# Performance work log

Hardware: AMD Instinct MI355X
Metric: run time of the kernel (lower is better)

## Reference

```python
import jax, jax.numpy as jnp
import numpy as np

N_TOKENS, D_MODEL, D_FF, N_EXPERTS, TOP_K = 4096, 2048, 1408, 8, 2


def setup_inputs() -> dict:
    key = jax.random.key(0)
    ks = jax.random.split(key, 6)
    s = 0.02
    return {
        "x": jax.random.normal(ks[0], (N_TOKENS, D_MODEL), jnp.float32),
        "topK_indices": jax.random.randint(ks[1], (N_TOKENS, TOP_K), 0, N_EXPERTS, jnp.int32),
        "topK_scores": jax.random.uniform(ks[2], (N_TOKENS, TOP_K), jnp.float32),
        "W_gate": jax.random.normal(ks[3], (N_EXPERTS, D_MODEL, D_FF), jnp.float32) * s,
        "W_up": jax.random.normal(ks[4], (N_EXPERTS, D_MODEL, D_FF), jnp.float32) * s,
        "W_down": jax.random.normal(ks[5], (N_EXPERTS, D_FF, D_MODEL), jnp.float32) * s,
    }


def reference(x, topK_indices, topK_scores, W_gate, W_up, W_down):
    # Combine weights: combine[n, e] = sum over k of score[n, k] where idx[n, k] == e.
    # Mathematically identical to the torch sort/split/index_add dispatch-combine
    # (with multiply_gate_scores=True), expressed densely for a clean jax baseline.
    n = x.shape[0]
    rows = jnp.arange(n)[:, None]  # [N, 1]
    combine = jnp.zeros((n, W_gate.shape[0]), x.dtype).at[rows, topK_indices].add(topK_scores)
    # Per-expert SwiGLU MLP (llama-moe LinearGLUExperts, bias-free).
    h = jax.nn.silu(jnp.einsum("nd,edh->enh", x, W_gate)) * jnp.einsum("nd,edh->enh", x, W_up)
    expert_out = jnp.einsum("enh,ehd->end", h, W_down)  # [E, N, D]
    y = jnp.einsum("ne,end->nd", combine, expert_out)  # weighted scatter-add combine
    return y
```

## Files before the change

kernel.cpp:

```cpp
#include <hip/hip_runtime.h>
#include <hip/hip_bf16.h>


#define NTOK 4096
#define DMODEL 2048
#define DFF 1408
#define NEXP 8
#define TOPK 2
#define NSLOT (NTOK * TOPK)
#define MAX_TILES 160
#define NTILE 40
#define NY1 11
#define NY2 8

typedef short bf16x8 __attribute__((ext_vector_type(8)));
typedef float f32x4 __attribute__((ext_vector_type(4)));

#define MFMA16(a, b, c) __builtin_amdgcn_mfma_f32_16x16x32_bf16(a, b, c, 0, 0, 0)

__device__ inline void async16(const void* g, void* l) {
    __builtin_amdgcn_global_load_lds(
        (const __attribute__((address_space(1))) void*)g,
        (__attribute__((address_space(3))) void*)l, 16, 0, 0);
}

__device__ inline int xcd_swz(int bid, int nblk) {
    int q = nblk >> 3, r = nblk & 7;
    int x = bid & 7, p = bid >> 3;
    return (x < r ? x * (q + 1) : r * (q + 1) + (x - r) * q) + p;
}

__global__ __launch_bounds__(256) void route_kernel(
    const int* __restrict__ idx, const float* __restrict__ scores,
    int* __restrict__ meta, int* __restrict__ slot_token, float* __restrict__ slot_score,
    int bm)
{
    __shared__ int counts[NEXP];
    __shared__ int cursor[NEXP];
    int t = threadIdx.x;
    if (t < NEXP) counts[t] = 0;
    __syncthreads();
    for (int i = t; i < NSLOT; i += 256) atomicAdd(&counts[idx[i]], 1);
    __syncthreads();
    if (t == 0) {
        int off = 0, nt = 0;
        for (int e = 0; e < NEXP; e++) {
            cursor[e] = off;
            int c = counts[e];
            for (int s = 0; s < c && nt < MAX_TILES; s += bm) {
                meta[1 + nt * 3 + 0] = e;
                meta[1 + nt * 3 + 1] = off + s;
                meta[1 + nt * 3 + 2] = min(bm, c - s);
                nt++;
            }
            off += c;
        }
        meta[0] = nt;
    }
    __syncthreads();
    for (int i = t; i < NSLOT; i += 256) {
        int e = idx[i];
        int pos = atomicAdd(&cursor[e], 1);
        slot_token[pos] = i / TOPK;
        slot_score[pos] = scores[i];
    }
}

__global__ __launch_bounds__(256) void convert_x(
    const float* __restrict__ x, __hip_bfloat16* __restrict__ xb)
{
    int i = blockIdx.x * 256 + threadIdx.x;
    float4 v = reinterpret_cast<const float4*>(x)[i];
    __hip_bfloat16 o[4] = {(__hip_bfloat16)v.x, (__hip_bfloat16)v.y,
                           (__hip_bfloat16)v.z, (__hip_bfloat16)v.w};
    *reinterpret_cast<uint2*>(&xb[(size_t)i * 4]) = *reinterpret_cast<uint2*>(o);
}

__global__ __launch_bounds__(256) void transpose_convert(
    const float* __restrict__ in, __hip_bfloat16* __restrict__ out, int R, int C)
{
    __shared__ __hip_bfloat16 t[64][72];
    const size_t base = (size_t)blockIdx.z * R * C;
    const int c0 = blockIdx.x * 64, r0 = blockIdx.y * 64;
    const int tid = threadIdx.x;
    const int rl = tid >> 4, c4 = (tid & 15) * 4;
    #pragma unroll
    for (int j = 0; j < 4; j++) {
        int r = rl + j * 16;
        float4 v = *reinterpret_cast<const float4*>(&in[base + (size_t)(r0 + r) * C + c0 + c4]);
        t[c4 + 0][r] = (__hip_bfloat16)v.x;
        t[c4 + 1][r] = (__hip_bfloat16)v.y;
        t[c4 + 2][r] = (__hip_bfloat16)v.z;
        t[c4 + 3][r] = (__hip_bfloat16)v.w;
    }
    __syncthreads();
    const int nl = tid >> 3, k8 = (tid & 7) * 8;
    #pragma unroll
    for (int j = 0; j < 2; j++) {
        int n = nl + j * 32;
        const uint* p = reinterpret_cast<const uint*>(&t[n][k8]);
        uint4 o = {p[0], p[1], p[2], p[3]};
        *reinterpret_cast<uint4*>(&out[base + (size_t)(c0 + n) * R + r0 + k8]) = o;
    }
}

__global__ __launch_bounds__(512, 2) void moe_gemm1_fast(
    const __hip_bfloat16* __restrict__ xb,
    const __hip_bfloat16* __restrict__ WgT, const __hip_bfloat16* __restrict__ WuT,
    const int* __restrict__ meta, const int* __restrict__ slot_token,
    __hip_bfloat16* __restrict__ h)
{
    const int swz = xcd_swz(blockIdx.x, NTILE * NY1);
    const int tile = swz / NY1, yb = swz % NY1;
    if (tile >= meta[0]) return;
    const int e = meta[1 + tile * 3], slot0 = meta[2 + tile * 3], rows = meta[3 + tile * 3];
    const int n0 = yb * 128;

    __shared__ __hip_bfloat16 As[2][256][64];
    __shared__ __hip_bfloat16 Bgs[2][128][64];
    __shared__ __hip_bfloat16 Bus[2][128][64];

    const int tid = threadIdx.x, lane = tid & 63, w = tid >> 6;
    const int wm = w >> 2, wn = w & 3, l15 = lane & 15, lg = lane >> 4;
    const int swb = l15 & 7;

    uint aoff[4], boff[2];
    #pragma unroll
    for (int i = 0; i < 4; i++) {
        int chunk = tid + i * 512;
        int r = chunk >> 3;
        int rc = r < rows ? r : rows - 1;
        int slot8 = (chunk & 7) ^ (r & 7);
        aoff[i] = (uint)(slot_token[slot0 + rc] * (DMODEL * 2) + slot8 * 16);
    }
    #pragma unroll
    for (int i = 0; i < 2; i++) {
        int chunk = tid + i * 512;
        int n = chunk >> 3;
        int slot8 = (chunk & 7) ^ (n & 7);
        boff[i] = (uint)((n0 + n) * (DMODEL * 2) + slot8 * 16);
    }
    const char* xbp = (const char*)xb;
    const char* wgp = (const char*)(WgT + (size_t)e * DFF * DMODEL);
    const char* wup = (const char*)(WuT + (size_t)e * DFF * DMODEL);

    f32x4 ag[8][2] = {};
    f32x4 au[8][2] = {};

    auto stage = [&](int kt, int buf) {
        const int kb = kt * 128;
        char* ab = (char*)As[buf]  + w * 1024;
        char* gb = (char*)Bgs[buf] + w * 1024;
        char* ub = (char*)Bus[buf] + w * 1024;
        #pragma unroll
        for (int i = 0; i < 4; i++) async16(xbp + aoff[i] + kb, ab + i * 8192);
        #pragma unroll
        for (int i = 0; i < 2; i++) {
            async16(wgp + boff[i] + kb, gb + i * 8192);
            async16(wup + boff[i] + kb, ub + i * 8192);
        }
    };

    constexpr int NT = DMODEL / 64;
    stage(0, 0);
    stage(1, 1);

    for (int kt = 0; kt < NT; ++kt) {
        const int cur = kt & 1;
        if (kt < NT - 1) asm volatile("s_waitcnt vmcnt(8)" ::: "memory");
        else             asm volatile("s_waitcnt vmcnt(0)" ::: "memory");
        __builtin_amdgcn_s_barrier();

        bf16x8 a[2][8], bg[2][2], bu[2][2];
        #pragma unroll
        for (int kk = 0; kk < 2; kk++) {
            const int cb = ((kk * 4 + lg) ^ swb) * 16;
            #pragma unroll
            for (int mf = 0; mf < 8; mf++)
                a[kk][mf] = *(const bf16x8*)((const char*)&As[cur][wm * 128 + mf * 16 + l15][0] + cb);
            #pragma unroll
            for (int nf = 0; nf < 2; nf++) {
                bg[kk][nf] = *(const bf16x8*)((const char*)&Bgs[cur][wn * 32 + nf * 16 + l15][0] + cb);
                bu[kk][nf] = *(const bf16x8*)((const char*)&Bus[cur][wn * 32 + nf * 16 + l15][0] + cb);
            }
        }
        asm volatile("s_waitcnt lgkmcnt(0)" ::: "memory");
        __builtin_amdgcn_s_barrier();
        if (kt + 2 < NT) stage(kt + 2, cur);

        __builtin_amdgcn_s_setprio(1);
        #pragma unroll
        for (int kk = 0; kk < 2; kk++)
            #pragma unroll
            for (int mf = 0; mf < 8; mf++)
                #pragma unroll
                for (int nf = 0; nf < 2; nf++) {
                    ag[mf][nf] = MFMA16(a[kk][mf], bg[kk][nf], ag[mf][nf]);
                    au[mf][nf] = MFMA16(a[kk][mf], bu[kk][nf], au[mf][nf]);
                }
        __builtin_amdgcn_s_setprio(0);
    }

    #pragma unroll
    for (int mf = 0; mf < 8; mf++) {
        #pragma unroll
        for (int j = 0; j < 4; j++) {
            int r = wm * 128 + mf * 16 + lg * 4 + j;
            if (r < rows) {
                size_t hrow = (size_t)(slot0 + r) * DFF + n0 + wn * 32;
                #pragma unroll
                for (int nf = 0; nf < 2; nf++) {
                    float g = ag[mf][nf][j], u = au[mf][nf][j];
                    float hv = g / (1.0f + __expf(-g)) * u;
                    h[hrow + nf * 16 + l15] = (__hip_bfloat16)hv;
                }
            }
        }
    }
}

__global__ __launch_bounds__(512, 2) void moe_gemm2_fast(
    const __hip_bfloat16* __restrict__ h, const __hip_bfloat16* __restrict__ WdT,
    const int* __restrict__ meta, const int* __restrict__ slot_token,
    const float* __restrict__ slot_score, float* __restrict__ out)
{
    const int swz = xcd_swz(blockIdx.x, NTILE * NY2);
    const int tile = swz / NY2, yb = swz % NY2;
    if (tile >= meta[0]) return;
    const int e = meta[1 + tile * 3], slot0 = meta[2 + tile * 3], rows = meta[3 + tile * 3];
    const int n0 = yb * 256;

    __shared__ __hip_bfloat16 Ah[2][256][64];
    __shared__ __hip_bfloat16 Bd[2][256][64];

    const int tid = threadIdx.x, lane = tid & 63, w = tid >> 6;
    const int wm = w >> 2, wn = w & 3, l15 = lane & 15, lg = lane >> 4;
    const int swb = l15 & 7;

    uint aoff[4], boff[4];
    #pragma unroll
    for (int i = 0; i < 4; i++) {
        int chunk = tid + i * 512;
        int r = chunk >> 3;
        int rc = r < rows ? r : rows - 1;
        int slot8 = (chunk & 7) ^ (r & 7);
        aoff[i] = (uint)((slot0 + rc) * (DFF * 2) + slot8 * 16);
        boff[i] = (uint)((n0 + r) * (DFF * 2) + slot8 * 16);
    }
    const char* hp  = (const char*)h;
    const char* wdp = (const char*)(WdT + (size_t)e * DMODEL * DFF);

    f32x4 acc[8][4] = {};

    auto stage = [&](int kt, int buf) {
        const int kb = kt * 128;
        char* ab = (char*)Ah[buf] + w * 1024;
        char* bb = (char*)Bd[buf] + w * 1024;
        #pragma unroll
        for (int i = 0; i < 4; i++) {
            async16(hp  + aoff[i] + kb, ab + i * 8192);
            async16(wdp + boff[i] + kb, bb + i * 8192);
        }
    };

    constexpr int NT = DFF / 64;
    stage(0, 0);
    stage(1, 1);

    for (int kt = 0; kt < NT; ++kt) {
        const int cur = kt & 1;
        if (kt < NT - 1) asm volatile("s_waitcnt vmcnt(8)" ::: "memory");
        else             asm volatile("s_waitcnt vmcnt(0)" ::: "memory");
        __builtin_amdgcn_s_barrier();

        bf16x8 a[2][8], b[2][4];
        #pragma unroll
        for (int kk = 0; kk < 2; kk++) {
            const int cb = ((kk * 4 + lg) ^ swb) * 16;
            #pragma unroll
            for (int mf = 0; mf < 8; mf++)
                a[kk][mf] = *(const bf16x8*)((const char*)&Ah[cur][wm * 128 + mf * 16 + l15][0] + cb);
            #pragma unroll
            for (int nf = 0; nf < 4; nf++)
                b[kk][nf] = *(const bf16x8*)((const char*)&Bd[cur][wn * 64 + nf * 16 + l15][0] + cb);
        }
        asm volatile("s_waitcnt lgkmcnt(0)" ::: "memory");
        __builtin_amdgcn_s_barrier();
        if (kt + 2 < NT) stage(kt + 2, cur);

        __builtin_amdgcn_s_setprio(1);
        #pragma unroll
        for (int kk = 0; kk < 2; kk++)
            #pragma unroll
            for (int mf = 0; mf < 8; mf++)
                #pragma unroll
                for (int nf = 0; nf < 4; nf++)
                    acc[mf][nf] = MFMA16(a[kk][mf], b[kk][nf], acc[mf][nf]);
        __builtin_amdgcn_s_setprio(0);
    }

    #pragma unroll
    for (int mf = 0; mf < 8; mf++) {
        #pragma unroll
        for (int j = 0; j < 4; j++) {
            int r = wm * 128 + mf * 16 + lg * 4 + j;
            if (r < rows) {
                int slot = slot0 + r;
                int tok = slot_token[slot];
                float s = slot_score[slot];
                float* orow = out + (size_t)tok * DMODEL + n0 + wn * 64;
                #pragma unroll
                for (int nf = 0; nf < 4; nf++)
                    atomicAdd(&orow[nf * 16 + l15], s * acc[mf][nf][j]);
            }
        }
    }
}

__global__ __launch_bounds__(256) void moe_gemm1(
    const float* __restrict__ x, const float* __restrict__ Wg, const float* __restrict__ Wu,
    const int* __restrict__ meta, const int* __restrict__ slot_token,
    __hip_bfloat16* __restrict__ h)
{
    int tile = blockIdx.x;
    if (tile >= meta[0]) return;
    const int e = meta[1 + tile * 3], slot0 = meta[2 + tile * 3], rows = meta[3 + tile * 3];
    const int n0 = blockIdx.y * 64;
    __shared__ __hip_bfloat16 As[64][72];
    __shared__ __hip_bfloat16 Bgs[64][72];
    __shared__ __hip_bfloat16 Bus[64][72];
    const int tid = threadIdx.x, lane = tid & 63, w = tid >> 6;
    const int wm = w >> 1, wn = w & 1, l15 = lane & 15, lg = lane >> 4;
    const float* __restrict__ WgE = Wg + (size_t)e * DMODEL * DFF;
    const float* __restrict__ WuE = Wu + (size_t)e * DMODEL * DFF;
    f32x4 acc_g[2][2] = {};
    f32x4 acc_u[2][2] = {};
    for (int k0 = 0; k0 < DMODEL; k0 += 64) {
        __syncthreads();
        #pragma unroll
        for (int j = 0; j < 4; j++) {
            int linear = tid + j * 256;
            int r = linear >> 4, c4 = (linear & 15) * 4;
            int tok = (r < rows) ? slot_token[slot0 + r] : 0;
            float4 v = *reinterpret_cast<const float4*>(&x[(size_t)tok * DMODEL + k0 + c4]);
            As[r][c4 + 0] = (__hip_bfloat16)v.x; As[r][c4 + 1] = (__hip_bfloat16)v.y;
            As[r][c4 + 2] = (__hip_bfloat16)v.z; As[r][c4 + 3] = (__hip_bfloat16)v.w;
        }
        #pragma unroll
        for (int j = 0; j < 4; j++) {
            int linear = tid + j * 256;
            int k = linear >> 4, n4 = (linear & 15) * 4;
            float4 vg = *reinterpret_cast<const float4*>(&WgE[(size_t)(k0 + k) * DFF + n0 + n4]);
            Bgs[n4 + 0][k] = (__hip_bfloat16)vg.x; Bgs[n4 + 1][k] = (__hip_bfloat16)vg.y;
            Bgs[n4 + 2][k] = (__hip_bfloat16)vg.z; Bgs[n4 + 3][k] = (__hip_bfloat16)vg.w;
            float4 vu = *reinterpret_cast<const float4*>(&WuE[(size_t)(k0 + k) * DFF + n0 + n4]);
            Bus[n4 + 0][k] = (__hip_bfloat16)vu.x; Bus[n4 + 1][k] = (__hip_bfloat16)vu.y;
            Bus[n4 + 2][k] = (__hip_bfloat16)vu.z; Bus[n4 + 3][k] = (__hip_bfloat16)vu.w;
        }
        __syncthreads();
        #pragma unroll
        for (int kk = 0; kk < 2; kk++) {
            bf16x8 a[2], bg[2], bu[2];
            #pragma unroll
            for (int mf = 0; mf < 2; mf++)
                a[mf] = *reinterpret_cast<const bf16x8*>(&As[wm * 32 + mf * 16 + l15][kk * 32 + lg * 8]);
            #pragma unroll
            for (int nf = 0; nf < 2; nf++) {
                bg[nf] = *reinterpret_cast<const bf16x8*>(&Bgs[wn * 32 + nf * 16 + l15][kk * 32 + lg * 8]);
                bu[nf] = *reinterpret_cast<const bf16x8*>(&Bus[wn * 32 + nf * 16 + l15][kk * 32 + lg * 8]);
            }
            #pragma unroll
            for (int mf = 0; mf < 2; mf++)
                #pragma unroll
                for (int nf = 0; nf < 2; nf++) {
                    acc_g[mf][nf] = MFMA16(a[mf], bg[nf], acc_g[mf][nf]);
                    acc_u[mf][nf] = MFMA16(a[mf], bu[nf], acc_u[mf][nf]);
                }
        }
    }
    #pragma unroll
    for (int mf = 0; mf < 2; mf++)
        #pragma unroll
        for (int nf = 0; nf < 2; nf++)
            #pragma unroll
            for (int j = 0; j < 4; j++) {
                int r = wm * 32 + mf * 16 + lg * 4 + j;
                int c = wn * 32 + nf * 16 + l15;
                if (r < rows) {
                    float g = acc_g[mf][nf][j], u = acc_u[mf][nf][j];
                    h[(size_t)(slot0 + r) * DFF + n0 + c] = (__hip_bfloat16)(g / (1.0f + __expf(-g)) * u);
                }
            }
}

__global__ __launch_bounds__(256) void moe_gemm2(
    const __hip_bfloat16* __restrict__ h, const float* __restrict__ Wd,
    const int* __restrict__ meta, const int* __restrict__ slot_token,
    const float* __restrict__ slot_score, float* __restrict__ out)
{
    int tile = blockIdx.x;
    if (tile >= meta[0]) return;
    const int e = meta[1 + tile * 3], slot0 = meta[2 + tile * 3], rows = meta[3 + tile * 3];
    const int n0 = blockIdx.y * 64;
    __shared__ __hip_bfloat16 As[64][72];
    __shared__ __hip_bfloat16 Bs[64][72];
    const int tid = threadIdx.x, lane = tid & 63, w = tid >> 6;
    const int wm = w >> 1, wn = w & 1, l15 = lane & 15, lg = lane >> 4;
    const float* __restrict__ WdE = Wd + (size_t)e * DFF * DMODEL;
    f32x4 acc[2][2] = {};
    for (int k0 = 0; k0 < DFF; k0 += 64) {
        __syncthreads();
        #pragma unroll
        for (int j = 0; j < 2; j++) {
            int linear = tid + j * 256;
            int r = linear >> 3, c8 = (linear & 7) * 8;
            bf16x8 v = *reinterpret_cast<const bf16x8*>(&h[(size_t)(slot0 + r) * DFF + k0 + c8]);
            *reinterpret_cast<bf16x8*>(&As[r][c8]) = v;
        }
        #pragma unroll
        for (int j = 0; j < 4; j++) {
            int linear = tid + j * 256;
            int k = linear >> 4, n4 = (linear & 15) * 4;
            float4 v = *reinterpret_cast<const float4*>(&WdE[(size_t)(k0 + k) * DMODEL + n0 + n4]);
            Bs[n4 + 0][k] = (__hip_bfloat16)v.x; Bs[n4 + 1][k] = (__hip_bfloat16)v.y;
            Bs[n4 + 2][k] = (__hip_bfloat16)v.z; Bs[n4 + 3][k] = (__hip_bfloat16)v.w;
        }
        __syncthreads();
        #pragma unroll
        for (int kk = 0; kk < 2; kk++) {
            bf16x8 a[2], b[2];
            #pragma unroll
            for (int mf = 0; mf < 2; mf++)
                a[mf] = *reinterpret_cast<const bf16x8*>(&As[wm * 32 + mf * 16 + l15][kk * 32 + lg * 8]);
            #pragma unroll
            for (int nf = 0; nf < 2; nf++)
                b[nf] = *reinterpret_cast<const bf16x8*>(&Bs[wn * 32 + nf * 16 + l15][kk * 32 + lg * 8]);
            #pragma unroll
            for (int mf = 0; mf < 2; mf++)
                #pragma unroll
                for (int nf = 0; nf < 2; nf++)
                    acc[mf][nf] = MFMA16(a[mf], b[nf], acc[mf][nf]);
        }
    }
    #pragma unroll
    for (int mf = 0; mf < 2; mf++)
        #pragma unroll
        for (int nf = 0; nf < 2; nf++)
            #pragma unroll
            for (int j = 0; j < 4; j++) {
                int r = wm * 32 + mf * 16 + lg * 4 + j;
                int c = wn * 32 + nf * 16 + l15;
                if (r < rows) {
                    int slot = slot0 + r;
                    atomicAdd(&out[(size_t)slot_token[slot] * DMODEL + n0 + c],
                              acc[mf][nf][j] * slot_score[slot]);
                }
            }
}

extern "C" void kernel_launch(void* const* d_in, const int* in_sizes, int n_in,
                              void* d_out, int out_size, void* d_ws, size_t ws_size,
                              hipStream_t stream) {
    const float* x      = (const float*)d_in[0];
    const int*   idx    = (const int*)d_in[1];
    const float* scores = (const float*)d_in[2];
    const float* Wg     = (const float*)d_in[3];
    const float* Wu     = (const float*)d_in[4];
    const float* Wd     = (const float*)d_in[5];
    float* out = (float*)d_out;

    char* ws = (char*)d_ws;
    int*   meta       = (int*)ws;
    int*   slot_token = (int*)(ws + 4096);
    float* slot_score = (float*)(ws + 4096 + 34816);

    const size_t XB_OFF = (size_t)1 << 20;
    const size_t HB_OFF = (size_t)20 << 20;
    const size_t WG_OFF = (size_t)44 << 20;
    const size_t WU_OFF = (size_t)92 << 20;
    const size_t WD_OFF = (size_t)140 << 20;
    const size_t NEED   = (size_t)187 << 20;
    const bool fast = ws_size >= NEED;

    hipMemsetAsync(d_out, 0, (size_t)NTOK * DMODEL * sizeof(float), stream);
    route_kernel<<<1, 256, 0, stream>>>(idx, scores, meta, slot_token, slot_score, fast ? 256 : 64);

    if (fast) {
        __hip_bfloat16* xb  = (__hip_bfloat16*)(ws + XB_OFF);
        __hip_bfloat16* hb  = (__hip_bfloat16*)(ws + HB_OFF);
        __hip_bfloat16* WgT = (__hip_bfloat16*)(ws + WG_OFF);
        __hip_bfloat16* WuT = (__hip_bfloat16*)(ws + WU_OFF);
        __hip_bfloat16* WdT = (__hip_bfloat16*)(ws + WD_OFF);

        dim3 td(DMODEL / 64, DFF / 64, NEXP);
        transpose_convert<<<td, 256, 0, stream>>>(Wd, WdT, DFF, DMODEL);
        dim3 tg(DFF / 64, DMODEL / 64, NEXP);
        transpose_convert<<<tg, 256, 0, stream>>>(Wg, WgT, DMODEL, DFF);
        transpose_convert<<<tg, 256, 0, stream>>>(Wu, WuT, DMODEL, DFF);
        convert_x<<<(NTOK * DMODEL / 4) / 256, 256, 0, stream>>>(x, xb);

        moe_gemm1_fast<<<NTILE * NY1, 512, 0, stream>>>(xb, WgT, WuT, meta, slot_token, hb);
        moe_gemm2_fast<<<NTILE * NY2, 512, 0, stream>>>(hb, WdT, meta, slot_token, slot_score, out);
    } else {
        __hip_bfloat16* hb = (__hip_bfloat16*)(ws + 81920);
        dim3 g1(NSLOT / 64 + NEXP, DFF / 64);
        moe_gemm1<<<g1, 256, 0, stream>>>(x, Wg, Wu, meta, slot_token, hb);
        dim3 g2(NSLOT / 64 + NEXP, DMODEL / 64);
        moe_gemm2<<<g2, 256, 0, stream>>>(hb, Wd, meta, slot_token, slot_score, out);
    }
}
```

Baseline: 373.3 us.

## Split K-half LDS loads to overlap MFMA; shrink GEMM2 tiles to 128x128

In both GEMM kernels the two k-halves of each LDS fragment load are split. The first half's MFMAs are issued as soon as its fragments arrive, while the second half is still loading, with the global stage of the next tile issued between them. GEMM2 is also retiled from 256x256 tiles with 512 threads to 128x128 tiles with 256 threads. Routing now builds a second tile-metadata table with 128-row tiles, giving more blocks and less row-padding waste for imbalanced experts. The smaller tiles lower reuse per block and increase the number of output atomics issued in parallel.

```diff
diff --git a/kernel.cpp b/kernel.cpp
--- a/kernel.cpp
+++ b/kernel.cpp
@@ -9,9 +9,10 @@
 #define TOPK 2
 #define NSLOT (NTOK * TOPK)
 #define MAX_TILES 160
-#define NTILE 40
+#define NTILE_A 40
+#define NTILE_B 72
 #define NY1 11
-#define NY2 8
+#define NY2 16
 
 typedef short bf16x8 __attribute__((ext_vector_type(8)));
 typedef float f32x4 __attribute__((ext_vector_type(4)));
@@ -32,8 +33,9 @@
 
 __global__ __launch_bounds__(256) void route_kernel(
     const int* __restrict__ idx, const float* __restrict__ scores,
-    int* __restrict__ meta, int* __restrict__ slot_token, float* __restrict__ slot_score,
-    int bm)
+    int* __restrict__ metaA, int* __restrict__ metaB,
+    int* __restrict__ slot_token, float* __restrict__ slot_score,
+    int bmA, int bmB)
 {
     __shared__ int counts[NEXP];
     __shared__ int cursor[NEXP];
@@ -47,15 +49,27 @@
         for (int e = 0; e < NEXP; e++) {
             cursor[e] = off;
             int c = counts[e];
-            for (int s = 0; s < c && nt < MAX_TILES; s += bm) {
-                meta[1 + nt * 3 + 0] = e;
-                meta[1 + nt * 3 + 1] = off + s;
-                meta[1 + nt * 3 + 2] = min(bm, c - s);
+            for (int s = 0; s < c && nt < MAX_TILES; s += bmA) {
+                metaA[1 + nt * 3 + 0] = e;
+                metaA[1 + nt * 3 + 1] = off + s;
+                metaA[1 + nt * 3 + 2] = min(bmA, c - s);
                 nt++;
             }
             off += c;
         }
-        meta[0] = nt;
+        metaA[0] = nt;
+        off = 0; nt = 0;
+        for (int e = 0; e < NEXP; e++) {
+            int c = counts[e];
+            for (int s = 0; s < c && nt < MAX_TILES; s += bmB) {
+                metaB[1 + nt * 3 + 0] = e;
+                metaB[1 + nt * 3 + 1] = off + s;
+                metaB[1 + nt * 3 + 2] = min(bmB, c - s);
+                nt++;
+            }
+            off += c;
+        }
+        metaB[0] = nt;
     }
     __syncthreads();
     for (int i = t; i < NSLOT; i += 256) {
@@ -110,7 +124,7 @@
     const int* __restrict__ meta, const int* __restrict__ slot_token,
     __hip_bfloat16* __restrict__ h)
 {
-    const int swz = xcd_swz(blockIdx.x, NTILE * NY1);
+    const int swz = xcd_swz(blockIdx.x, NTILE_A * NY1);
     const int tile = swz / NY1, yb = swz % NY1;
     if (tile >= meta[0]) return;
     const int e = meta[1 + tile * 3], slot0 = meta[2 + tile * 3], rows = meta[3 + tile * 3];
@@ -171,33 +185,49 @@
         else             asm volatile("s_waitcnt vmcnt(0)" ::: "memory");
         __builtin_amdgcn_s_barrier();
 
-        bf16x8 a[2][8], bg[2][2], bu[2][2];
-        #pragma unroll
-        for (int kk = 0; kk < 2; kk++) {
-            const int cb = ((kk * 4 + lg) ^ swb) * 16;
-            #pragma unroll
-            for (int mf = 0; mf < 8; mf++)
-                a[kk][mf] = *(const bf16x8*)((const char*)&As[cur][wm * 128 + mf * 16 + l15][0] + cb);
+        const int cb0 = (lg ^ swb) * 16;
+        const int cb1 = ((4 + lg) ^ swb) * 16;
+        bf16x8 a0[8], bg0[2], bu0[2], a1[8], bg1[2], bu1[2];
+        #pragma unroll
+        for (int mf = 0; mf < 8; mf++)
+            a0[mf] = *(const bf16x8*)((const char*)&As[cur][wm * 128 + mf * 16 + l15][0] + cb0);
+        #pragma unroll
+        for (int nf = 0; nf < 2; nf++) {
+            bg0[nf] = *(const bf16x8*)((const char*)&Bgs[cur][wn * 32 + nf * 16 + l15][0] + cb0);
+            bu0[nf] = *(const bf16x8*)((const char*)&Bus[cur][wn * 32 + nf * 16 + l15][0] + cb0);
+        }
+        __builtin_amdgcn_sched_barrier(0);
+        #pragma unroll
+        for (int mf = 0; mf < 8; mf++)
+            a1[mf] = *(const bf16x8*)((const char*)&As[cur][wm * 128 + mf * 16 + l15][0] + cb1);
+        #pragma unroll
+        for (int nf = 0; nf < 2; nf++) {
+            bg1[nf] = *(const bf16x8*)((const char*)&Bgs[cur][wn * 32 + nf * 16 + l15][0] + cb1);
+            bu1[nf] = *(const bf16x8*)((const char*)&Bus[cur][wn * 32 + nf * 16 + l15][0] + cb1);
+        }
+        asm volatile("s_waitcnt lgkmcnt(12)" ::: "memory");
+        __builtin_amdgcn_sched_barrier(0);
+        __builtin_amdgcn_s_setprio(1);
+        #pragma unroll
+        for (int mf = 0; mf < 8; mf++)
             #pragma unroll
             for (int nf = 0; nf < 2; nf++) {
-                bg[kk][nf] = *(const bf16x8*)((const char*)&Bgs[cur][wn * 32 + nf * 16 + l15][0] + cb);
-                bu[kk][nf] = *(const bf16x8*)((const char*)&Bus[cur][wn * 32 + nf * 16 + l15][0] + cb);
-            }
-        }
+                ag[mf][nf] = MFMA16(a0[mf], bg0[nf], ag[mf][nf]);
+                au[mf][nf] = MFMA16(a0[mf], bu0[nf], au[mf][nf]);
+            }
+        __builtin_amdgcn_s_setprio(0);
         asm volatile("s_waitcnt lgkmcnt(0)" ::: "memory");
+        __builtin_amdgcn_sched_barrier(0);
         __builtin_amdgcn_s_barrier();
         if (kt + 2 < NT) stage(kt + 2, cur);
-
         __builtin_amdgcn_s_setprio(1);
         #pragma unroll
-        for (int kk = 0; kk < 2; kk++)
-            #pragma unroll
-            for (int mf = 0; mf < 8; mf++)
-                #pragma unroll
-                for (int nf = 0; nf < 2; nf++) {
-                    ag[mf][nf] = MFMA16(a[kk][mf], bg[kk][nf], ag[mf][nf]);
-                    au[mf][nf] = MFMA16(a[kk][mf], bu[kk][nf], au[mf][nf]);
-                }
+        for (int mf = 0; mf < 8; mf++)
+            #pragma unroll
+            for (int nf = 0; nf < 2; nf++) {
+                ag[mf][nf] = MFMA16(a1[mf], bg1[nf], ag[mf][nf]);
+                au[mf][nf] = MFMA16(a1[mf], bu1[nf], au[mf][nf]);
+            }
         __builtin_amdgcn_s_setprio(0);
     }
 
@@ -219,28 +249,28 @@
     }
 }
 
-__global__ __launch_bounds__(512, 2) void moe_gemm2_fast(
+__global__ __launch_bounds__(256, 2) void moe_gemm2_fast(
     const __hip_bfloat16* __restrict__ h, const __hip_bfloat16* __restrict__ WdT,
     const int* __restrict__ meta, const int* __restrict__ slot_token,
     const float* __restrict__ slot_score, float* __restrict__ out)
 {
-    const int swz = xcd_swz(blockIdx.x, NTILE * NY2);
+    const int swz = xcd_swz(blockIdx.x, NTILE_B * NY2);
     const int tile = swz / NY2, yb = swz % NY2;
     if (tile >= meta[0]) return;
     const int e = meta[1 + tile * 3], slot0 = meta[2 + tile * 3], rows = meta[3 + tile * 3];
-    const int n0 = yb * 256;
-
-    __shared__ __hip_bfloat16 Ah[2][256][64];
-    __shared__ __hip_bfloat16 Bd[2][256][64];
+    const int n0 = yb * 128;
+
+    __shared__ __hip_bfloat16 Ah[2][128][64];
+    __shared__ __hip_bfloat16 Bd[2][128][64];
 
     const int tid = threadIdx.x, lane = tid & 63, w = tid >> 6;
-    const int wm = w >> 2, wn = w & 3, l15 = lane & 15, lg = lane >> 4;
+    const int wm = w >> 1, wn = w & 1, l15 = lane & 15, lg = lane >> 4;
     const int swb = l15 & 7;
 
     uint aoff[4], boff[4];
     #pragma unroll
     for (int i = 0; i < 4; i++) {
-        int chunk = tid + i * 512;
+        int chunk = tid + i * 256;
         int r = chunk >> 3;
         int rc = r < rows ? r : rows - 1;
         int slot8 = (chunk & 7) ^ (r & 7);
@@ -250,7 +280,7 @@
     const char* hp  = (const char*)h;
     const char* wdp = (const char*)(WdT + (size_t)e * DMODEL * DFF);
 
-    f32x4 acc[8][4] = {};
+    f32x4 acc[4][4] = {};
 
     auto stage = [&](int kt, int buf) {
         const int kb = kt * 128;
@@ -258,8 +288,8 @@
         char* bb = (char*)Bd[buf] + w * 1024;
         #pragma unroll
         for (int i = 0; i < 4; i++) {
-            async16(hp  + aoff[i] + kb, ab + i * 8192);
-            async16(wdp + boff[i] + kb, bb + i * 8192);
+            async16(hp  + aoff[i] + kb, ab + i * 4096);
+            async16(wdp + boff[i] + kb, bb + i * 4096);
         }
     };
 
@@ -273,37 +303,47 @@
         else             asm volatile("s_waitcnt vmcnt(0)" ::: "memory");
         __builtin_amdgcn_s_barrier();
 
-        bf16x8 a[2][8], b[2][4];
-        #pragma unroll
-        for (int kk = 0; kk < 2; kk++) {
-            const int cb = ((kk * 4 + lg) ^ swb) * 16;
-            #pragma unroll
-            for (int mf = 0; mf < 8; mf++)
-                a[kk][mf] = *(const bf16x8*)((const char*)&Ah[cur][wm * 128 + mf * 16 + l15][0] + cb);
+        const int cb0 = (lg ^ swb) * 16;
+        const int cb1 = ((4 + lg) ^ swb) * 16;
+        bf16x8 a0[4], b0[4], a1[4], b1[4];
+        #pragma unroll
+        for (int mf = 0; mf < 4; mf++) {
+            a0[mf] = *(const bf16x8*)((const char*)&Ah[cur][wm * 64 + mf * 16 + l15][0] + cb0);
+            b0[mf] = *(const bf16x8*)((const char*)&Bd[cur][wn * 64 + mf * 16 + l15][0] + cb0);
+        }
+        __builtin_amdgcn_sched_barrier(0);
+        #pragma unroll
+        for (int mf = 0; mf < 4; mf++) {
+            a1[mf] = *(const bf16x8*)((const char*)&Ah[cur][wm * 64 + mf * 16 + l15][0] + cb1);
+            b1[mf] = *(const bf16x8*)((const char*)&Bd[cur][wn * 64 + mf * 16 + l15][0] + cb1);
+        }
+        asm volatile("s_waitcnt lgkmcnt(8)" ::: "memory");
+        __builtin_amdgcn_sched_barrier(0);
+        __builtin_amdgcn_s_setprio(1);
+        #pragma unroll
+        for (int mf = 0; mf < 4; mf++)
             #pragma unroll
             for (int nf = 0; nf < 4; nf++)
-                b[kk][nf] = *(const bf16x8*)((const char*)&Bd[cur][wn * 64 + nf * 16 + l15][0] + cb);
-        }
+                acc[mf][nf] = MFMA16(a0[mf], b0[nf], acc[mf][nf]);
+        __builtin_amdgcn_s_setprio(0);
         asm volatile("s_waitcnt lgkmcnt(0)" ::: "memory");
+        __builtin_amdgcn_sched_barrier(0);
         __builtin_amdgcn_s_barrier();
         if (kt + 2 < NT) stage(kt + 2, cur);
-
         __builtin_amdgcn_s_setprio(1);
         #pragma unroll
-        for (int kk = 0; kk < 2; kk++)
-            #pragma unroll
-            for (int mf = 0; mf < 8; mf++)
-                #pragma unroll
-                for (int nf = 0; nf < 4; nf++)
-                    acc[mf][nf] = MFMA16(a[kk][mf], b[kk][nf], acc[mf][nf]);
+        for (int mf = 0; mf < 4; mf++)
+            #pragma unroll
+            for (int nf = 0; nf < 4; nf++)
+                acc[mf][nf] = MFMA16(a1[mf], b1[nf], acc[mf][nf]);
         __builtin_amdgcn_s_setprio(0);
     }
 
     #pragma unroll
-    for (int mf = 0; mf < 8; mf++) {
+    for (int mf = 0; mf < 4; mf++) {
         #pragma unroll
         for (int j = 0; j < 4; j++) {
-            int r = wm * 128 + mf * 16 + lg * 4 + j;
+            int r = wm * 64 + mf * 16 + lg * 4 + j;
             if (r < rows) {
                 int slot = slot0 + r;
                 int tok = slot_token[slot];
@@ -470,9 +510,10 @@
     float* out = (float*)d_out;
 
     char* ws = (char*)d_ws;
-    int*   meta       = (int*)ws;
-    int*   slot_token = (int*)(ws + 4096);
-    float* slot_score = (float*)(ws + 4096 + 34816);
+    int*   metaA      = (int*)ws;
+    int*   metaB      = (int*)(ws + 4096);
+    int*   slot_token = (int*)(ws + 8192);
+    float* slot_score = (float*)(ws + 8192 + 32768);
 
     const size_t XB_OFF = (size_t)1 << 20;
     const size_t HB_OFF = (size_t)20 << 20;
@@ -483,7 +524,8 @@
     const bool fast = ws_size >= NEED;
 
     hipMemsetAsync(d_out, 0, (size_t)NTOK * DMODEL * sizeof(float), stream);
-    route_kernel<<<1, 256, 0, stream>>>(idx, scores, meta, slot_token, slot_score, fast ? 256 : 64);
+    route_kernel<<<1, 256, 0, stream>>>(idx, scores, metaA, metaB, slot_token, slot_score,
+                                        fast ? 256 : 64, fast ? 128 : 64);
 
     if (fast) {
         __hip_bfloat16* xb  = (__hip_bfloat16*)(ws + XB_OFF);
@@ -499,13 +541,13 @@
         transpose_convert<<<tg, 256, 0, stream>>>(Wu, WuT, DMODEL, DFF);
         convert_x<<<(NTOK * DMODEL / 4) / 256, 256, 0, stream>>>(x, xb);
 
-        moe_gemm1_fast<<<NTILE * NY1, 512, 0, stream>>>(xb, WgT, WuT, meta, slot_token, hb);
-        moe_gemm2_fast<<<NTILE * NY2, 512, 0, stream>>>(hb, WdT, meta, slot_token, slot_score, out);
+        moe_gemm1_fast<<<NTILE_A * NY1, 512, 0, stream>>>(xb, WgT, WuT, metaA, slot_token, hb);
+        moe_gemm2_fast<<<NTILE_B * NY2, 256, 0, stream>>>(hb, WdT, metaB, slot_token, slot_score, out);
     } else {
-        __hip_bfloat16* hb = (__hip_bfloat16*)(ws + 81920);
+        __hip_bfloat16* hb = (__hip_bfloat16*)(ws + HB_OFF);
         dim3 g1(NSLOT / 64 + NEXP, DFF / 64);
-        moe_gemm1<<<g1, 256, 0, stream>>>(x, Wg, Wu, meta, slot_token, hb);
+        moe_gemm1<<<g1, 256, 0, stream>>>(x, Wg, Wu, metaA, slot_token, hb);
         dim3 g2(NSLOT / 64 + NEXP, DMODEL / 64);
-        moe_gemm2<<<g2, 256, 0, stream>>>(hb, Wd, meta, slot_token, slot_score, out);
-    }
-}
+        moe_gemm2<<<g2, 256, 0, stream>>>(hb, Wd, metaB, slot_token, slot_score, out);
+    }
+}
```

New measurement: 361.4 us. 1.03x faster.
